# Kernel optimization log

Measured on AMD Instinct MI355X. Metric: run time of the kernel, lower is better.

The kernel has to match this reference:

```python
import jax, jax.numpy as jnp
import numpy as np

N = 4096
D = 256
H = 8
HD = D // H
EPS = 1e-5
NEG = -1e9


def layer_norm(x, g, b):
    mu = jnp.mean(x, axis=-1, keepdims=True)
    var = jnp.mean(jnp.square(x - mu), axis=-1, keepdims=True)
    return (x - mu) * jax.lax.rsqrt(var + EPS) * g + b


def setup_inputs() -> dict:
    key = jax.random.key(0)
    ks = jax.random.split(key, 12)
    s = 1.0 / np.sqrt(D)
    inp = {
        "x": jax.random.normal(ks[0], (N, D), dtype=jnp.float32),
        "adj": jax.random.randint(ks[1], (N, N), 0, 2, dtype=jnp.int32),
        "Wq": jax.random.uniform(ks[2], (D, D), jnp.float32, -s, s),
        "Wk": jax.random.uniform(ks[3], (D, D), jnp.float32, -s, s),
        "Wv": jax.random.uniform(ks[4], (D, D), jnp.float32, -s, s),
        "bq": jnp.zeros((D,), jnp.float32),
        "bk": jnp.zeros((D,), jnp.float32),
        "bv": jnp.zeros((D,), jnp.float32),
        "Wo": jax.random.uniform(ks[5], (D, D), jnp.float32, -s, s),
        "bo": jnp.zeros((D,), jnp.float32),
        "g1": jnp.ones((D,), jnp.float32),
        "beta1": jnp.zeros((D,), jnp.float32),
        "W1": jax.random.uniform(ks[6], (2 * D, D), jnp.float32, -s, s),
        "b1": jnp.zeros((2 * D,), jnp.float32),
        "W2": jax.random.uniform(ks[7], (D, 2 * D), jnp.float32, -1.0 / np.sqrt(2 * D), 1.0 / np.sqrt(2 * D)),
        "b2": jnp.zeros((D,), jnp.float32),
        "g2": jnp.ones((D,), jnp.float32),
        "beta2": jnp.zeros((D,), jnp.float32),
    }
    return inp


def reference(x, adj, Wq, Wk, Wv, bq, bk, bv, Wo, bo, g1, beta1, W1, b1, W2, b2, g2, beta2):
    n = adj.shape[0]
    # allowed = adj + I > 0 ; attention only over neighbors + self-loop
    allowed = (adj + jnp.eye(n, dtype=adj.dtype)) > 0  # (n, n) bool

    q = (x @ Wq.T + bq).reshape(n, H, HD)
    k = (x @ Wk.T + bk).reshape(n, H, HD)
    v = (x @ Wv.T + bv).reshape(n, H, HD)

    scale = 1.0 / np.sqrt(HD)
    scores = jnp.einsum('nhd,mhd->hnm', q, k) * scale  # (H, n, n)
    scores = jnp.where(allowed[None, :, :], scores, NEG)
    attn = jax.nn.softmax(scores, axis=-1)
    o = jnp.einsum('hnm,mhd->nhd', attn, v).reshape(n, D)
    h = o @ Wo.T + bo

    x = layer_norm(x + h, g1, beta1)
    ffn = jax.nn.relu(x @ W1.T + b1) @ W2.T + b2
    x = layer_norm(x + ffn, g2, beta2)
    return x
```

## Files before the change

kernel.cpp:

```cpp
#include <hip/hip_runtime.h>
#include <hip/hip_bf16.h>

typedef __attribute__((ext_vector_type(4))) float f32x4;
typedef __attribute__((ext_vector_type(8))) short s16x8;

#define NROWS 4096
#define DMODEL 256
#define NHEAD 8
#define HDIM 32
#define PSTRIDE 72
#define OSTRIDE 33
#define M2C 24.0f
#define NM (NROWS * DMODEL)
#define SA_S 264
#define SH_S 268
#define SY_S 264
#define SR_S 520

__device__ __forceinline__ short bf16r(float f) {
    union { float f; unsigned u; } v; v.f = f;
    unsigned r = v.u + 0x7fffu + ((v.u >> 16) & 1u);
    return (short)(r >> 16);
}

__device__ __forceinline__ float fexp2(float x) {
    float r;
    asm("v_exp_f32 %0, %1" : "=v"(r) : "v"(x));
    return r;
}

__device__ __forceinline__ unsigned pk_bf16(float a, float b) {
#if __has_builtin(__builtin_amdgcn_cvt_pk_bf16_f32)
    typedef __bf16 bf2 __attribute__((ext_vector_type(2)));
    union { bf2 h; unsigned u; } c;
    c.h = __builtin_amdgcn_cvt_pk_bf16_f32(a, b);
    return c.u;
#else
    return (unsigned)(unsigned short)bf16r(a) | ((unsigned)(unsigned short)bf16r(b) << 16);
#endif
}

__device__ __forceinline__ s16x8 pack8(float4 a, float4 b) {
    s16x8 r;
    r[0] = bf16r(a.x); r[1] = bf16r(a.y); r[2] = bf16r(a.z); r[3] = bf16r(a.w);
    r[4] = bf16r(b.x); r[5] = bf16r(b.y); r[6] = bf16r(b.z); r[7] = bf16r(b.w);
    return r;
}

__global__ __launch_bounds__(256) void qkvprep_kernel(
        const float* __restrict__ X,
        const float* __restrict__ Wq, const float* __restrict__ Wk,
        const float* __restrict__ Wv,
        const float* __restrict__ bq, const float* __restrict__ bk,
        const float* __restrict__ bv,
        const int* __restrict__ adj, unsigned* __restrict__ mask,
        const float* __restrict__ Wo, const float* __restrict__ W1,
        const float* __restrict__ W2, short* __restrict__ Wb,
        short* __restrict__ Qb, short* __restrict__ Kb,
        short* __restrict__ Vtb) {
    const int b = blockIdx.x;
    const int tid = threadIdx.x;
    const int lane = tid & 63;
    if (b < 768) {
        const int wv = tid >> 6;
        const int quad = lane >> 4, col = lane & 15;
        const int bx = b & 63, by = b >> 6;
        const int o0 = by * 64;
        const int z = o0 >> 8;
        const float* Wsrc = (z == 0) ? Wq : (z == 1 ? Wk : Wv);
        const float* bias = (z == 0) ? bq : (z == 1 ? bk : bv);
        const int ow0 = o0 & 255;
        const int n0 = bx * 64 + wv * 16;
        const float QSC = 0.25505653437397888f;

        f32x4 zero = {0.f, 0.f, 0.f, 0.f};
        f32x4 acc[4] = {zero, zero, zero, zero};
        const float* ap = X + (size_t)(n0 + col) * DMODEL + quad * 8;
#pragma unroll
        for (int k0 = 0; k0 < DMODEL; k0 += 32) {
            float4 a0 = *(const float4*)(ap + k0);
            float4 a1 = *(const float4*)(ap + k0 + 4);
            s16x8 af = pack8(a0, a1);
#pragma unroll
            for (int t = 0; t < 4; ++t) {
                const float* wp = Wsrc + (size_t)(ow0 + t * 16 + col) * DMODEL + quad * 8 + k0;
                s16x8 bf = pack8(*(const float4*)wp, *(const float4*)(wp + 4));
                acc[t] = __builtin_amdgcn_mfma_f32_16x16x32_bf16(af, bf, acc[t], 0, 0, 0);
            }
        }
#pragma unroll
        for (int t = 0; t < 4; ++t) {
            const int oo = ow0 + t * 16 + col;
            float bvv = bias[oo];
#pragma unroll
            for (int r = 0; r < 4; ++r) {
                int n = n0 + quad * 4 + r;
                float v = acc[t][r] + bvv;
                if (z == 0)      Qb[(size_t)n * DMODEL + oo] = bf16r(v * QSC);
                else if (z == 1) Kb[(size_t)(oo >> 5) * NROWS * HDIM + (size_t)n * HDIM + (oo & 31)] = bf16r(v);
                else             Vtb[(size_t)oo * NROWS + n] = bf16r(v);
            }
        }
    } else if (b < 2816) {
        const int waveid = (b - 768) * 4 + (tid >> 6);
#pragma unroll
        for (int i = 0; i < 32; ++i) {
            const int task = waveid + i * 8192;
            const int row = task >> 6, chunk = task & 63;
            const int c = chunk * 64 + lane;
            int a = adj[(size_t)row * NROWS + c];
            unsigned long long m = __ballot(a > 0 || c == row);
            if (lane == 0)      mask[row * 128 + chunk * 2]     = (unsigned)m;
            else if (lane == 1) mask[row * 128 + chunk * 2 + 1] = (unsigned)(m >> 32);
        }
    } else {
        int i = (b - 2816) * 2048 + tid * 8;
        const float* src; int off;
        if (i < 65536)       { src = Wo; off = i; }
        else if (i < 196608) { src = W1; off = i - 65536; }
        else                 { src = W2; off = i - 196608; }
        float4 a = *(const float4*)(src + off);
        float4 c = *(const float4*)(src + off + 4);
        *(s16x8*)(Wb + i) = pack8(a, c);
    }
}

__global__ __launch_bounds__(256) void attn_kernel(const short* __restrict__ Qb,
                                                   const short* __restrict__ Kb,
                                                   const short* __restrict__ Vtb,
                                                   const unsigned* __restrict__ mask,
                                                   float* __restrict__ Opart,
                                                   float* __restrict__ lpart) {
    __shared__ union {
        short sP[2][16 * PSTRIDE];
        float sO[HDIM][OSTRIDE];
    } u[4];
    __shared__ float sl[4][32];

    const int tid = threadIdx.x;
    const int wv = tid >> 6, lane = tid & 63;
    const int quad = lane >> 4, col = lane & 15;
    const int khalf = blockIdx.x & 1;
    const int h = (blockIdx.x >> 1) & 7;
    const int q0 = (blockIdx.x >> 4) * 32;
    const int kw = khalf * 2048 + wv * 512;

    s16x8 qf[2];
    qf[0] = *(const s16x8*)(Qb + (size_t)(q0 + col) * DMODEL + h * HDIM + quad * 8);
    qf[1] = *(const s16x8*)(Qb + (size_t)(q0 + 16 + col) * DMODEL + h * HDIM + quad * 8);

    const short* kp  = Kb + (size_t)h * NROWS * HDIM + (size_t)(kw + col) * HDIM + quad * 8;
    const short* vp0 = Vtb + (size_t)(h * HDIM + col) * NROWS + kw + quad * 8;
    const short* vp1 = vp0 + (size_t)16 * NROWS;
    const unsigned* mp0 = mask + (size_t)(q0 + col) * 128 + (kw >> 5);
    const unsigned* mp1 = mp0 + 16 * 128;

    const short onev = (col == 0) ? (short)0x3F80 : (short)0;
    const s16x8 ones = {onev, onev, onev, onev, onev, onev, onev, onev};

    f32x4 zero = {0.f, 0.f, 0.f, 0.f};
    f32x4 acc[2][2] = {{zero, zero}, {zero, zero}};
    f32x4 lacc[2] = {zero, zero};
    const f32x4 cinit = {-M2C, -M2C, -M2C, -M2C};

#pragma unroll 2
    for (int it = 0; it < 8; ++it) {
        const short* k = kp + it * 64 * HDIM;
        s16x8 kf0 = *(const s16x8*)(k);
        s16x8 kf1 = *(const s16x8*)(k + 16 * HDIM);
        s16x8 kf2 = *(const s16x8*)(k + 32 * HDIM);
        s16x8 kf3 = *(const s16x8*)(k + 48 * HDIM);
        uint2 w0 = *(const uint2*)(mp0 + it * 2);
        uint2 w1 = *(const uint2*)(mp1 + it * 2);
        const short* v0 = vp0 + it * 64;
        const short* v1 = vp1 + it * 64;
        s16x8 vf00 = *(const s16x8*)(v0);
        s16x8 vf01 = *(const s16x8*)(v0 + 32);
        s16x8 vf10 = *(const s16x8*)(v1);
        s16x8 vf11 = *(const s16x8*)(v1 + 32);

#pragma unroll
        for (int qs = 0; qs < 2; ++qs) {
            unsigned wlo = (qs ? w1.x : w0.x) >> (quad * 4);
            unsigned whi = (qs ? w1.y : w0.y) >> (quad * 4);
            f32x4 st[4];
            st[0] = __builtin_amdgcn_mfma_f32_16x16x32_bf16(kf0, qf[qs], cinit, 0, 0, 0);
            st[1] = __builtin_amdgcn_mfma_f32_16x16x32_bf16(kf1, qf[qs], cinit, 0, 0, 0);
            st[2] = __builtin_amdgcn_mfma_f32_16x16x32_bf16(kf2, qf[qs], cinit, 0, 0, 0);
            st[3] = __builtin_amdgcn_mfma_f32_16x16x32_bf16(kf3, qf[qs], cinit, 0, 0, 0);

            float p[4][4];
#pragma unroll
            for (int t = 0; t < 4; ++t) {
                unsigned wm = (t < 2) ? wlo : whi;
#pragma unroll
                for (int r = 0; r < 4; ++r) {
                    float e = fexp2(st[t][r]);
                    bool ok = (wm & (1u << ((t & 1) * 16 + r))) != 0u;
                    p[t][r] = ok ? e : 0.f;
                }
            }

            short* pb = &u[wv].sP[qs][0];
#pragma unroll
            for (int t = 0; t < 4; ++t) {
                uint2 pr;
                pr.x = pk_bf16(p[t][0], p[t][1]);
                pr.y = pk_bf16(p[t][2], p[t][3]);
                *(uint2*)(pb + col * PSTRIDE + t * 16 + quad * 4) = pr;
            }
            s16x8 pb0 = *(const s16x8*)(pb + col * PSTRIDE + quad * 8);
            s16x8 pb1 = *(const s16x8*)(pb + col * PSTRIDE + 32 + quad * 8);

            acc[qs][0] = __builtin_amdgcn_mfma_f32_16x16x32_bf16(vf00, pb0, acc[qs][0], 0, 0, 0);
            acc[qs][0] = __builtin_amdgcn_mfma_f32_16x16x32_bf16(vf01, pb1, acc[qs][0], 0, 0, 0);
            acc[qs][1] = __builtin_amdgcn_mfma_f32_16x16x32_bf16(vf10, pb0, acc[qs][1], 0, 0, 0);
            acc[qs][1] = __builtin_amdgcn_mfma_f32_16x16x32_bf16(vf11, pb1, acc[qs][1], 0, 0, 0);
            lacc[qs] = __builtin_amdgcn_mfma_f32_16x16x32_bf16(ones, pb0, lacc[qs], 0, 0, 0);
            lacc[qs] = __builtin_amdgcn_mfma_f32_16x16x32_bf16(ones, pb1, lacc[qs], 0, 0, 0);
        }
    }

#pragma unroll
    for (int qs = 0; qs < 2; ++qs) {
        if (lane < 16) sl[wv][qs * 16 + col] = lacc[qs][0];
#pragma unroll
        for (int rr = 0; rr < 4; ++rr) {
            u[wv].sO[quad * 4 + rr][qs * 16 + col]      = acc[qs][0][rr];
            u[wv].sO[16 + quad * 4 + rr][qs * 16 + col] = acc[qs][1][rr];
        }
    }
    __syncthreads();

    const int q = tid >> 3, hd0 = (tid & 7) * 4;
    float l = sl[0][q] + sl[1][q] + sl[2][q] + sl[3][q];
    float4 ov;
    ov.x = u[0].sO[hd0][q]     + u[1].sO[hd0][q]     + u[2].sO[hd0][q]     + u[3].sO[hd0][q];
    ov.y = u[0].sO[hd0 + 1][q] + u[1].sO[hd0 + 1][q] + u[2].sO[hd0 + 1][q] + u[3].sO[hd0 + 1][q];
    ov.z = u[0].sO[hd0 + 2][q] + u[1].sO[hd0 + 2][q] + u[2].sO[hd0 + 2][q] + u[3].sO[hd0 + 2][q];
    ov.w = u[0].sO[hd0 + 3][q] + u[1].sO[hd0 + 3][q] + u[2].sO[hd0 + 3][q] + u[3].sO[hd0 + 3][q];
    *(float4*)(Opart + (size_t)khalf * NM + (size_t)(q0 + q) * DMODEL + h * HDIM + hd0) = ov;
    if ((tid & 7) == 0) lpart[khalf * NROWS * NHEAD + (q0 + q) * NHEAD + h] = l;
}

__global__ __launch_bounds__(256) void mega_kernel(
        const float* __restrict__ Opart, const float* __restrict__ lpart,
        const float* __restrict__ X,
        const short* __restrict__ Wob, const short* __restrict__ W1b,
        const short* __restrict__ W2b,
        const float* __restrict__ bo,
        const float* __restrict__ g1, const float* __restrict__ be1,
        const float* __restrict__ b1, const float* __restrict__ b2,
        const float* __restrict__ g2, const float* __restrict__ be2,
        float* __restrict__ out) {
    __shared__ union { short sA[16 * SA_S]; short sR[16 * SR_S]; } uu;
    __shared__ float sH[16 * SH_S];
    __shared__ short sY[16 * SY_S];

    const int tid = threadIdx.x;
    const int wv = tid >> 6, lane = tid & 63;
    const int quad = lane >> 4, col = lane & 15;
    const int n0 = blockIdx.x * 16;
    const int rr_ = tid >> 4, cg = tid & 15;
    const int n_ln = n0 + rr_;
    f32x4 zero = {0.f, 0.f, 0.f, 0.f};

    {
        const int head = cg >> 1;
        float li = 1.f / (lpart[(size_t)n_ln * NHEAD + head] +
                          lpart[(size_t)NROWS * NHEAD + (size_t)n_ln * NHEAD + head]);
        const float* p0 = Opart + (size_t)n_ln * DMODEL + cg * 16;
        const float* p1 = p0 + NM;
        short* dst = &uu.sA[rr_ * SA_S + cg * 16];
#pragma unroll
        for (int j = 0; j < 4; ++j) {
            float4 a = ((const float4*)p0)[j];
            float4 b = ((const float4*)p1)[j];
            uint2 w;
            w.x = pk_bf16((a.x + b.x) * li, (a.y + b.y) * li);
            w.y = pk_bf16((a.z + b.z) * li, (a.w + b.w) * li);
            *(uint2*)(dst + j * 4) = w;
        }
    }
    __syncthreads();

    {
        const int o0 = wv * 64;
        f32x4 acc[4] = {zero, zero, zero, zero};
#pragma unroll
        for (int k0 = 0; k0 < DMODEL; k0 += 32) {
            s16x8 af = *(const s16x8*)&uu.sA[col * SA_S + k0 + quad * 8];
#pragma unroll
            for (int t = 0; t < 4; ++t) {
                s16x8 bf = *(const s16x8*)(Wob + (size_t)(o0 + t * 16 + col) * DMODEL + k0 + quad * 8);
                acc[t] = __builtin_amdgcn_mfma_f32_16x16x32_bf16(af, bf, acc[t], 0, 0, 0);
            }
        }
#pragma unroll
        for (int t = 0; t < 4; ++t) {
            int o = o0 + t * 16 + col;
            float bv = bo[o];
#pragma unroll
            for (int r = 0; r < 4; ++r)
                sH[(quad * 4 + r) * SH_S + o] = acc[t][r] + bv;
        }
    }
    __syncthreads();

    float y1v[16];
    {
        const float* xp = X + (size_t)n_ln * DMODEL + cg * 16;
        float v[16];
        float s = 0.f;
#pragma unroll
        for (int j = 0; j < 4; ++j) {
            float4 xv = ((const float4*)xp)[j];
            float4 hv = *(const float4*)&sH[rr_ * SH_S + cg * 16 + j * 4];
            v[j * 4 + 0] = xv.x + hv.x; v[j * 4 + 1] = xv.y + hv.y;
            v[j * 4 + 2] = xv.z + hv.z; v[j * 4 + 3] = xv.w + hv.w;
            s += v[j * 4] + v[j * 4 + 1] + v[j * 4 + 2] + v[j * 4 + 3];
        }
#pragma unroll
        for (int m = 1; m < 16; m <<= 1) s += __shfl_xor(s, m, 64);
        float mean = s * (1.f / 256.f);
        float q = 0.f;
#pragma unroll
        for (int i = 0; i < 16; ++i) { v[i] -= mean; q += v[i] * v[i]; }
#pragma unroll
        for (int m = 1; m < 16; m <<= 1) q += __shfl_xor(q, m, 64);
        float rstd = rsqrtf(q * (1.f / 256.f) + 1e-5f);
        const float* gp = g1 + cg * 16;
        const float* bp = be1 + cg * 16;
        short* dst = &sY[rr_ * SY_S + cg * 16];
#pragma unroll
        for (int j = 0; j < 4; ++j) {
            float4 gv = ((const float4*)gp)[j];
            float4 bev = ((const float4*)bp)[j];
            float a0 = v[j * 4 + 0] * rstd * gv.x + bev.x;
            float a1 = v[j * 4 + 1] * rstd * gv.y + bev.y;
            float a2 = v[j * 4 + 2] * rstd * gv.z + bev.z;
            float a3 = v[j * 4 + 3] * rstd * gv.w + bev.w;
            y1v[j * 4 + 0] = a0; y1v[j * 4 + 1] = a1;
            y1v[j * 4 + 2] = a2; y1v[j * 4 + 3] = a3;
            uint2 w;
            w.x = pk_bf16(a0, a1);
            w.y = pk_bf16(a2, a3);
            *(uint2*)(dst + j * 4) = w;
        }
    }
    __syncthreads();

    {
        const int o0 = wv * 128;
        f32x4 acc[8] = {zero, zero, zero, zero, zero, zero, zero, zero};
#pragma unroll
        for (int k0 = 0; k0 < DMODEL; k0 += 32) {
            s16x8 af = *(const s16x8*)&sY[col * SY_S + k0 + quad * 8];
#pragma unroll
            for (int t = 0; t < 8; ++t) {
                s16x8 bf = *(const s16x8*)(W1b + (size_t)(o0 + t * 16 + col) * DMODEL + k0 + quad * 8);
                acc[t] = __builtin_amdgcn_mfma_f32_16x16x32_bf16(af, bf, acc[t], 0, 0, 0);
            }
        }
#pragma unroll
        for (int t = 0; t < 8; ++t) {
            int o = o0 + t * 16 + col;
            float bv = b1[o];
#pragma unroll
            for (int r = 0; r < 4; ++r)
                uu.sR[(quad * 4 + r) * SR_S + o] = bf16r(fmaxf(acc[t][r] + bv, 0.f));
        }
    }
    __syncthreads();

    {
        const int o0 = wv * 64;
        f32x4 acc[4] = {zero, zero, zero, zero};
#pragma unroll
        for (int k0 = 0; k0 < 512; k0 += 32) {
            s16x8 af = *(const s16x8*)&uu.sR[col * SR_S + k0 + quad * 8];
#pragma unroll
            for (int t = 0; t < 4; ++t) {
                s16x8 bf = *(const s16x8*)(W2b + (size_t)(o0 + t * 16 + col) * 512 + k0 + quad * 8);
                acc[t] = __builtin_amdgcn_mfma_f32_16x16x32_bf16(af, bf, acc[t], 0, 0, 0);
            }
        }
#pragma unroll
        for (int t = 0; t < 4; ++t) {
            int o = o0 + t * 16 + col;
            float bv = b2[o];
#pragma unroll
            for (int r = 0; r < 4; ++r)
                sH[(quad * 4 + r) * SH_S + o] = acc[t][r] + bv;
        }
    }
    __syncthreads();

    {
        float v[16];
        float s = 0.f;
#pragma unroll
        for (int j = 0; j < 4; ++j) {
            float4 hv = *(const float4*)&sH[rr_ * SH_S + cg * 16 + j * 4];
            v[j * 4 + 0] = y1v[j * 4 + 0] + hv.x; v[j * 4 + 1] = y1v[j * 4 + 1] + hv.y;
            v[j * 4 + 2] = y1v[j * 4 + 2] + hv.z; v[j * 4 + 3] = y1v[j * 4 + 3] + hv.w;
            s += v[j * 4] + v[j * 4 + 1] + v[j * 4 + 2] + v[j * 4 + 3];
        }
#pragma unroll
        for (int m = 1; m < 16; m <<= 1) s += __shfl_xor(s, m, 64);
        float mean = s * (1.f / 256.f);
        float q = 0.f;
#pragma unroll
        for (int i = 0; i < 16; ++i) { v[i] -= mean; q += v[i] * v[i]; }
#pragma unroll
        for (int m = 1; m < 16; m <<= 1) q += __shfl_xor(q, m, 64);
        float rstd = rsqrtf(q * (1.f / 256.f) + 1e-5f);
        const float* gp = g2 + cg * 16;
        const float* bp = be2 + cg * 16;
        float* op = out + (size_t)n_ln * DMODEL + cg * 16;
#pragma unroll
        for (int j = 0; j < 4; ++j) {
            float4 gv = ((const float4*)gp)[j];
            float4 bev = ((const float4*)bp)[j];
            float4 y;
            y.x = v[j * 4 + 0] * rstd * gv.x + bev.x;
            y.y = v[j * 4 + 1] * rstd * gv.y + bev.y;
            y.z = v[j * 4 + 2] * rstd * gv.z + bev.z;
            y.w = v[j * 4 + 3] * rstd * gv.w + bev.w;
            ((float4*)op)[j] = y;
        }
    }
}

extern "C" void kernel_launch(void* const* d_in, const int* in_sizes, int n_in,
                              void* d_out, int out_size, void* d_ws, size_t ws_size,
                              hipStream_t stream) {
    const float* x   = (const float*)d_in[0];
    const int*   adj = (const int*)d_in[1];
    const float* Wq  = (const float*)d_in[2];
    const float* Wk  = (const float*)d_in[3];
    const float* Wv  = (const float*)d_in[4];
    const float* bq  = (const float*)d_in[5];
    const float* bk  = (const float*)d_in[6];
    const float* bv  = (const float*)d_in[7];
    const float* Wo  = (const float*)d_in[8];
    const float* bo  = (const float*)d_in[9];
    const float* g1  = (const float*)d_in[10];
    const float* be1 = (const float*)d_in[11];
    const float* W1  = (const float*)d_in[12];
    const float* b1  = (const float*)d_in[13];
    const float* W2  = (const float*)d_in[14];
    const float* b2  = (const float*)d_in[15];
    const float* g2  = (const float*)d_in[16];
    const float* be2 = (const float*)d_in[17];
    float* out = (float*)d_out;

    char* p = (char*)d_ws;
    unsigned* mask = (unsigned*)p; p += (size_t)NROWS * 128 * 4;
    short* Wb    = (short*)p;      p += (size_t)327680 * 2;
    short* Qb    = (short*)p;      p += (size_t)NM * 2;
    short* Kb    = (short*)p;      p += (size_t)NM * 2;
    short* Vtb   = (short*)p;      p += (size_t)NM * 2;
    float* Opart = (float*)p;      p += (size_t)2 * NM * 4;
    float* lpart = (float*)p;      p += (size_t)2 * NROWS * NHEAD * 4;

    qkvprep_kernel<<<dim3(2976), dim3(256), 0, stream>>>(
        x, Wq, Wk, Wv, bq, bk, bv, adj, mask, Wo, W1, W2, Wb, Qb, Kb, Vtb);
    attn_kernel<<<dim3(2048), dim3(256), 0, stream>>>(Qb, Kb, Vtb, mask, Opart, lpart);
    mega_kernel<<<dim3(256), dim3(256), 0, stream>>>(
        Opart, lpart, x, Wb, Wb + 65536, Wb + 196608,
        bo, g1, be1, b1, b2, g2, be2, out);
}
```

Baseline: 240.8 us.

## Vectorize adjacency mask build and compute softmax row sums with shuffles

The mask-building stage now has each lane load int4 chunks of the adjacency matrix and combine the 4-bit nibbles through xor shuffles, replacing one-element-per-lane ballots. In attention, the row-sum denominators are accumulated in fp32 registers and reduced across quads with shuffles, instead of two extra MFMA ops against a ones vector per step. The key loop is also changed from unroll 2 to unroll 1. The denominator is now summed from fp32 probabilities rather than bf16-rounded ones, which slightly changes numerics. Less unrolling may reduce overlap of loads with compute.

```diff
diff --git a/kernel.cpp b/kernel.cpp
--- a/kernel.cpp
+++ b/kernel.cpp
@@ -103,15 +103,28 @@
         }
     } else if (b < 2816) {
         const int waveid = (b - 768) * 4 + (tid >> 6);
-#pragma unroll
-        for (int i = 0; i < 32; ++i) {
+        int4 av[8];
+        int rows[8], segs[8];
+#pragma unroll
+        for (int i = 0; i < 8; ++i) {
             const int task = waveid + i * 8192;
-            const int row = task >> 6, chunk = task & 63;
-            const int c = chunk * 64 + lane;
-            int a = adj[(size_t)row * NROWS + c];
-            unsigned long long m = __ballot(a > 0 || c == row);
-            if (lane == 0)      mask[row * 128 + chunk * 2]     = (unsigned)m;
-            else if (lane == 1) mask[row * 128 + chunk * 2 + 1] = (unsigned)(m >> 32);
+            rows[i] = task >> 4; segs[i] = task & 15;
+            av[i] = *(const int4*)(adj + (size_t)rows[i] * NROWS + segs[i] * 256 + lane * 4);
+        }
+#pragma unroll
+        for (int i = 0; i < 8; ++i) {
+            const int row = rows[i];
+            const int c0 = segs[i] * 256 + lane * 4;
+            unsigned nib = (unsigned)(av[i].x > 0 || c0 == row)
+                         | ((unsigned)(av[i].y > 0 || c0 + 1 == row) << 1)
+                         | ((unsigned)(av[i].z > 0 || c0 + 2 == row) << 2)
+                         | ((unsigned)(av[i].w > 0 || c0 + 3 == row) << 3);
+            unsigned v = nib << ((lane & 7) * 4);
+            v |= __shfl_xor((int)v, 1, 64);
+            v |= __shfl_xor((int)v, 2, 64);
+            v |= __shfl_xor((int)v, 4, 64);
+            if ((lane & 7) == 0)
+                mask[row * 128 + segs[i] * 8 + (lane >> 3)] = v;
         }
     } else {
         int i = (b - 2816) * 2048 + tid * 8;
@@ -155,15 +168,12 @@
     const unsigned* mp0 = mask + (size_t)(q0 + col) * 128 + (kw >> 5);
     const unsigned* mp1 = mp0 + 16 * 128;
 
-    const short onev = (col == 0) ? (short)0x3F80 : (short)0;
-    const s16x8 ones = {onev, onev, onev, onev, onev, onev, onev, onev};
-
     f32x4 zero = {0.f, 0.f, 0.f, 0.f};
     f32x4 acc[2][2] = {{zero, zero}, {zero, zero}};
-    f32x4 lacc[2] = {zero, zero};
+    float rs[2] = {0.f, 0.f};
     const f32x4 cinit = {-M2C, -M2C, -M2C, -M2C};
 
-#pragma unroll 2
+#pragma unroll 1
     for (int it = 0; it < 8; ++it) {
         const short* k = kp + it * 64 * HDIM;
         s16x8 kf0 = *(const s16x8*)(k);
@@ -190,6 +200,7 @@
             st[3] = __builtin_amdgcn_mfma_f32_16x16x32_bf16(kf3, qf[qs], cinit, 0, 0, 0);
 
             float p[4][4];
+            float r0 = 0.f;
 #pragma unroll
             for (int t = 0; t < 4; ++t) {
                 unsigned wm = (t < 2) ? wlo : whi;
@@ -198,8 +209,10 @@
                     float e = fexp2(st[t][r]);
                     bool ok = (wm & (1u << ((t & 1) * 16 + r))) != 0u;
                     p[t][r] = ok ? e : 0.f;
+                    r0 += p[t][r];
                 }
             }
+            rs[qs] += r0;
 
             short* pb = &u[wv].sP[qs][0];
 #pragma unroll
@@ -216,14 +229,15 @@
             acc[qs][0] = __builtin_amdgcn_mfma_f32_16x16x32_bf16(vf01, pb1, acc[qs][0], 0, 0, 0);
             acc[qs][1] = __builtin_amdgcn_mfma_f32_16x16x32_bf16(vf10, pb0, acc[qs][1], 0, 0, 0);
             acc[qs][1] = __builtin_amdgcn_mfma_f32_16x16x32_bf16(vf11, pb1, acc[qs][1], 0, 0, 0);
-            lacc[qs] = __builtin_amdgcn_mfma_f32_16x16x32_bf16(ones, pb0, lacc[qs], 0, 0, 0);
-            lacc[qs] = __builtin_amdgcn_mfma_f32_16x16x32_bf16(ones, pb1, lacc[qs], 0, 0, 0);
         }
     }
 
 #pragma unroll
     for (int qs = 0; qs < 2; ++qs) {
-        if (lane < 16) sl[wv][qs * 16 + col] = lacc[qs][0];
+        float r = rs[qs];
+        r += __shfl_xor(r, 16, 64);
+        r += __shfl_xor(r, 32, 64);
+        if (lane < 16) sl[wv][qs * 16 + col] = r;
 #pragma unroll
         for (int rr = 0; rr < 4; ++rr) {
             u[wv].sO[quad * 4 + rr][qs * 16 + col]      = acc[qs][0][rr];
```

New measurement: 237.5 us. Within noise of the previous version (-1.4%).
